# Performance work log

Measured on AMD Instinct MI355X. Metric: run time of the kernel, lower is better.

The kernel has to match this reference:

```python
import jax, jax.numpy as jnp
import numpy as np

B, S, D, H, DH = 2, 2048, 1024, 16, 64
LN_EPS = 1e-5

def _layernorm(x, g, b):
    mu = jnp.mean(x, axis=-1, keepdims=True)
    var = jnp.mean(jnp.square(x - mu), axis=-1, keepdims=True)
    return (x - mu) * jax.lax.rsqrt(var + LN_EPS) * g + b

def setup_inputs() -> dict:
    key = jax.random.key(0)
    ks = jax.random.split(key, 12)
    s = 0.02
    return {
        'x': jax.random.normal(ks[0], (B, S, D), jnp.float32),
        'attention_mask': jnp.zeros((B, S), jnp.bool_),
        'Wq': jax.random.normal(ks[1], (H, D, DH), jnp.float32) * s,
        'bq': jnp.zeros((H, DH), jnp.float32),
        'Wk': jax.random.normal(ks[2], (H, D, DH), jnp.float32) * s,
        'bk': jnp.zeros((H, DH), jnp.float32),
        'Wv': jax.random.normal(ks[3], (H, D, DH), jnp.float32) * s,
        'bv': jnp.zeros((H, DH), jnp.float32),
        'ln_g': jnp.ones((D,), jnp.float32),
        'ln_b': jnp.zeros((D,), jnp.float32),
        'W1': jax.random.normal(ks[4], (D, 4 * D), jnp.float32) * s,
        'b1': jnp.zeros((4 * D,), jnp.float32),
        'W2': jax.random.normal(ks[5], (4 * D, D), jnp.float32) * s,
        'b2': jnp.zeros((D,), jnp.float32),
    }

def reference(x, attention_mask, Wq, bq, Wk, bk, Wv, bv, ln_g, ln_b, W1, b1, W2, b2):
    # NOTE: source has a typo bug ('attentoin_score'), so the attention_mask is
    # computed-then-discarded; softmax is applied to the UNMASKED scaled scores.
    dh = Wq.shape[-1]
    q = jnp.einsum('bsd,hde->bhse', x, Wq) + bq[:, None, :]  # [B,H,S,dh]
    k = jnp.einsum('bsd,hde->bhse', x, Wk) + bk[:, None, :]
    v = jnp.einsum('bsd,hde->bhse', x, Wv) + bv[:, None, :]
    scores = jnp.einsum('bhse,bhte->bhst', q, k) / jnp.sqrt(jnp.float32(dh))
    attn = jax.nn.softmax(scores, axis=-1)
    o = jnp.einsum('bhst,bhte->bhse', attn, v)  # [B,H,S,dh]
    b_, h_, s_, e_ = o.shape
    # concat heads along last dim == transpose then reshape
    mha = jnp.transpose(o, (0, 2, 1, 3)).reshape(b_, s_, h_ * e_)
    h1 = _layernorm(x + mha, ln_g, ln_b)
    ffn = jax.nn.relu(h1 @ W1 + b1) @ W2 + b2
    return _layernorm(h1 + ffn, ln_g, ln_b)
```

## Files before the change

kernel.cpp:

```cpp
#include <hip/hip_runtime.h>

#define DEVI __device__ __forceinline__

typedef __attribute__((ext_vector_type(8))) __bf16 bf16x8;
typedef __attribute__((ext_vector_type(4))) float f32x4;
typedef __attribute__((ext_vector_type(4))) unsigned short u16x4;
typedef __attribute__((ext_vector_type(8))) unsigned short u16x8;

static DEVI unsigned short f2bf(float f) {
  unsigned int i = __float_as_uint(f);
  i += 0x7fffu + ((i >> 16) & 1u);
  return (unsigned short)(i >> 16);
}

static DEVI unsigned short f2bfh(float f) {
  union { __bf16 h; unsigned short u; } c;
  c.h = (__bf16)f;
  return c.u;
}

static DEVI float bf2f(unsigned short u) {
  return __uint_as_float((unsigned int)u << 16);
}

static DEVI f32x4 mfma16x16x32(bf16x8 a, bf16x8 b, f32x4 c) {
  return __builtin_amdgcn_mfma_f32_16x16x32_bf16(a, b, c, 0, 0, 0);
}

static DEVI void async_ld16(const void* g, void* lds) {
  __builtin_amdgcn_global_load_lds(
      (const __attribute__((address_space(1))) void*)g,
      (__attribute__((address_space(3))) void*)lds, 16, 0, 0);
}

template <int OUT_MODE, bool RELU>
static DEVI void gemm256_core(const unsigned short* __restrict__ A, int lda,
                              const unsigned short* __restrict__ Bt, int ldb,
                              int m0, int n0, const float* __restrict__ bias,
                              void* __restrict__ Cp, int ldc,
                              const float* __restrict__ bq,
                              const float* __restrict__ bk,
                              const float* __restrict__ bv,
                              unsigned short* __restrict__ qo,
                              unsigned short* __restrict__ ko,
                              unsigned short* __restrict__ vo) {
  constexpr int NKT = 16;
  __shared__ __align__(16) unsigned short As[2][16384];
  __shared__ __align__(16) unsigned short Bs[2][16384];

  const int tid = threadIdx.x;
  const int w = tid >> 6, l = tid & 63;
  const int lr = l & 15, lq = l >> 4;
  const int wm = w >> 2, wn = w & 3;

  const int srow = tid >> 3;
  const int scol = ((tid & 7) ^ (srow & 7)) << 3;
  const unsigned short* sA = A + (size_t)(m0 + srow) * lda + scol;
  const unsigned short* sB = Bt + (size_t)(n0 + srow) * ldb + scol;
  unsigned short* dA = &As[0][0] + w * 512;
  unsigned short* dB = &Bs[0][0] + w * 512;

  auto stA = [&](int c, int h, int kb) {
    const unsigned short* s = sA + (size_t)h * 128 * lda + kb;
    unsigned short* d = dA + c * 16384 + h * 8192;
    async_ld16(s, d);
    async_ld16(s + (size_t)64 * lda, d + 4096);
  };
  auto stB = [&](int c, int h, int kb) {
    const unsigned short* s = sB + (size_t)h * 128 * ldb + kb;
    unsigned short* d = dB + c * 16384 + h * 8192;
    async_ld16(s, d);
    async_ld16(s + (size_t)64 * ldb, d + 4096);
  };

  stA(0, 0, 0); stB(0, 0, 0); stB(0, 1, 0); stA(0, 1, 0);
  stA(1, 0, 64); stB(1, 0, 64); stB(1, 1, 64);

  f32x4 acc[8][4];
#pragma unroll
  for (int i = 0; i < 8; ++i)
#pragma unroll
    for (int j = 0; j < 4; ++j) acc[i][j] = (f32x4){0.f, 0.f, 0.f, 0.f};

  const int frow = wm * 16 + lr;
  const int brow = wn * 16 + lr;
  const int g0 = (lq ^ (lr & 7)) << 3;
  const int g1 = ((4 + lq) ^ (lr & 7)) << 3;

  bf16x8 af[4][2], bf[2][2][2];

  auto mfma_quad = [&](int qm, int qn) {
    __builtin_amdgcn_s_setprio(1);
#pragma unroll
    for (int m = 0; m < 4; ++m)
#pragma unroll
      for (int n = 0; n < 2; ++n) {
        f32x4 t = acc[qm * 4 + m][qn * 2 + n];
        t = mfma16x16x32(af[m][0], bf[qn][n][0], t);
        t = mfma16x16x32(af[m][1], bf[qn][n][1], t);
        acc[qm * 4 + m][qn * 2 + n] = t;
      }
    __builtin_amdgcn_s_setprio(0);
  };

  asm volatile("s_waitcnt vmcnt(6)");
  __builtin_amdgcn_sched_barrier(0);
  __builtin_amdgcn_s_barrier();

  for (int kt = 0; kt < NKT; ++kt) {
    __builtin_amdgcn_sched_barrier(0);
    const int c = kt & 1;
    const unsigned short* Ac = &As[c][0];
    const unsigned short* Bc = &Bs[c][0];
    const int kb1 = (kt + 1) * 64, kb2 = (kt + 2) * 64;

#pragma unroll
    for (int m = 0; m < 4; ++m) {
      const unsigned short* p = Ac + (frow + m * 32) * 64;
      af[m][0] = *(const bf16x8*)(p + g0);
      af[m][1] = *(const bf16x8*)(p + g1);
    }
#pragma unroll
    for (int n = 0; n < 2; ++n) {
      const unsigned short* p = Bc + (brow + n * 64) * 64;
      bf[0][n][0] = *(const bf16x8*)(p + g0);
      bf[0][n][1] = *(const bf16x8*)(p + g1);
    }
    if (kt + 1 < NKT) stA(c ^ 1, 1, kb1);
    __builtin_amdgcn_s_barrier();
    asm volatile("s_waitcnt lgkmcnt(0)");
    __builtin_amdgcn_sched_barrier(0);
    mfma_quad(0, 0);
    __builtin_amdgcn_s_barrier();

#pragma unroll
    for (int n = 0; n < 2; ++n) {
      const unsigned short* p = Bc + (128 + brow + n * 64) * 64;
      bf[1][n][0] = *(const bf16x8*)(p + g0);
      bf[1][n][1] = *(const bf16x8*)(p + g1);
    }
    if (kt + 2 < NKT) stA(c, 0, kb2);
    __builtin_amdgcn_s_barrier();
    asm volatile("s_waitcnt lgkmcnt(0)");
    __builtin_amdgcn_sched_barrier(0);
    mfma_quad(0, 1);
    __builtin_amdgcn_s_barrier();

#pragma unroll
    for (int m = 0; m < 4; ++m) {
      const unsigned short* p = Ac + (128 + frow + m * 32) * 64;
      af[m][0] = *(const bf16x8*)(p + g0);
      af[m][1] = *(const bf16x8*)(p + g1);
    }
    if (kt + 2 < NKT) stB(c, 0, kb2);
    __builtin_amdgcn_s_barrier();
    asm volatile("s_waitcnt lgkmcnt(0)");
    __builtin_amdgcn_sched_barrier(0);
    mfma_quad(1, 0);
    __builtin_amdgcn_s_barrier();

    if (kt + 2 < NKT) stB(c, 1, kb2);
    __builtin_amdgcn_s_barrier();
    asm volatile("s_waitcnt lgkmcnt(0)");
    __builtin_amdgcn_sched_barrier(0);
    mfma_quad(1, 1);
    if (kt < NKT - 2)
      asm volatile("s_waitcnt vmcnt(6)");
    else
      asm volatile("s_waitcnt vmcnt(0)");
    __builtin_amdgcn_sched_barrier(0);
    __builtin_amdgcn_s_barrier();
  }

#pragma unroll
  for (int qm = 0; qm < 2; ++qm)
#pragma unroll
    for (int m = 0; m < 4; ++m) {
      const int grow = m0 + qm * 128 + wm * 16 + m * 32 + lq * 4;
#pragma unroll
      for (int qn = 0; qn < 2; ++qn)
#pragma unroll
        for (int n = 0; n < 2; ++n) {
          const int gcol = n0 + qn * 128 + wn * 16 + n * 64 + lr;
          const f32x4 av = acc[qm * 4 + m][qn * 2 + n];
          if (OUT_MODE == 2) {
            const int which = gcol >> 10;
            const int h = (gcol >> 6) & 15;
            const int e = gcol & 63;
            const float* bp = (which == 0) ? bq : (which == 1) ? bk : bv;
            const float bvv = bp[gcol & 1023];
#pragma unroll
            for (int r = 0; r < 4; ++r) {
              const int row = grow + r;
              const int b_ = row >> 11, s_ = row & 2047;
              const size_t base = (size_t)((b_ << 4) + h) * 131072;
              const float val = av[r] + bvv;
              if (which == 0) {
                qo[base + (size_t)s_ * 64 + e] = f2bf(val);
              } else if (which == 1) {
                const int o = e >> 3;
                const int pos = (((o ^ (s_ & 7)) << 3) | (e & 7));
                ko[base + (size_t)s_ * 64 + pos] = f2bf(val * 0.18033688011112f);
              } else {
                const int t = s_ >> 6, k64 = s_ & 63;
                const int kap = (k64 & 15) * 4 + (k64 >> 4);
                const int pos = (((kap >> 3) ^ (e & 7)) << 3) | (kap & 7);
                vo[base + (size_t)e * 2048 + t * 64 + pos] = f2bf(val);
              }
            }
          } else if (OUT_MODE == 3) {
#pragma unroll
            for (int r = 0; r < 4; ++r)
              ((unsigned short*)Cp)[(size_t)(grow + r) * ldc + gcol] =
                  f2bf(av[r]);
          } else {
            const float bvv = bias[gcol];
#pragma unroll
            for (int r = 0; r < 4; ++r) {
              float val = av[r] + bvv;
              if (RELU) val = fmaxf(val, 0.f);
              ((unsigned short*)Cp)[(size_t)(grow + r) * ldc + gcol] = f2bf(val);
            }
          }
        }
    }
}

__global__ __launch_bounds__(512, 2) void k_gemm_qkv(
    const unsigned short* __restrict__ xb, const unsigned short* __restrict__ Wt,
    const float* __restrict__ bq, const float* __restrict__ bk,
    const float* __restrict__ bv, unsigned short* __restrict__ qo,
    unsigned short* __restrict__ ko, unsigned short* __restrict__ vo) {
  const int bid = blockIdx.x;
  const int xcd = bid & 7, idx = bid >> 3;
  const int mt = (xcd >> 1) * 4 + idx / 6;
  const int nt = (xcd & 1) * 6 + idx % 6;
  gemm256_core<2, false>(xb, 1024, Wt, 1024, mt * 256, nt * 256, nullptr,
                         nullptr, 0, bq, bk, bv, qo, ko, vo);
}

__global__ __launch_bounds__(512, 2) void k_ffn1(
    const unsigned short* __restrict__ h1b, const unsigned short* __restrict__ W1t,
    const float* __restrict__ b1, unsigned short* __restrict__ f1) {
  const int bid = blockIdx.x;
  const int xcd = bid & 7, idx = bid >> 3;
  const int mt = (xcd >> 1) * 4 + (idx >> 3);
  const int nt = (xcd & 1) * 8 + (idx & 7);
  gemm256_core<1, true>(h1b, 1024, W1t, 1024, mt * 256, nt * 256, b1, f1, 4096,
                        nullptr, nullptr, nullptr, nullptr, nullptr, nullptr);
}

__global__ __launch_bounds__(512, 2) void k_ffn2(
    const unsigned short* __restrict__ f1, const unsigned short* __restrict__ W2t,
    unsigned short* __restrict__ pbase) {
  const int z = blockIdx.z;
  unsigned short* p = pbase + (size_t)z * 4194304;
  const int bid = blockIdx.x;
  const int xcd = bid & 7, idx = bid >> 3;
  const int mt = xcd * 2 + (idx >> 2);
  const int nt = idx & 3;
  gemm256_core<3, false>(f1 + z * 1024, 4096, W2t + z * 1024, 4096, mt * 256,
                         nt * 256, nullptr, p, 1024, nullptr, nullptr, nullptr,
                         nullptr, nullptr, nullptr);
}

static DEVI void tr64(const float* __restrict__ s, int sld,
                      unsigned short* __restrict__ d, int dld) {
  __shared__ float t[64][65];
  const int tr = threadIdx.x >> 4;
  const int tc4 = (threadIdx.x & 15) * 4;
#pragma unroll
  for (int i = 0; i < 4; ++i) {
    f32x4 v = *(const f32x4*)(s + (size_t)(i * 16 + tr) * sld + tc4);
#pragma unroll
    for (int j = 0; j < 4; ++j) t[i * 16 + tr][tc4 + j] = v[j];
  }
  __syncthreads();
#pragma unroll
  for (int i = 0; i < 4; ++i) {
    const int c = i * 16 + tr;
    u16x4 pk;
#pragma unroll
    for (int j = 0; j < 4; ++j) pk[j] = f2bf(t[tc4 + j][c]);
    *(u16x4*)(d + (size_t)c * dld + tc4) = pk;
  }
}

__global__ __launch_bounds__(256) void k_prep(
    const float* __restrict__ x, const float* __restrict__ Wq,
    const float* __restrict__ Wk, const float* __restrict__ Wv,
    const float* __restrict__ W1, const float* __restrict__ W2,
    unsigned short* __restrict__ xb, unsigned short* __restrict__ wqkvt,
    unsigned short* __restrict__ w1t, unsigned short* __restrict__ w2t) {
  const int bid = blockIdx.x;
  if (bid < 1024) {
    const size_t i0 = ((size_t)bid * 256 + threadIdx.x) * 16;
#pragma unroll
    for (int c = 0; c < 4; ++c) {
      f32x4 v = *(const f32x4*)(x + i0 + c * 4);
      u16x4 pk;
#pragma unroll
      for (int j = 0; j < 4; ++j) pk[j] = f2bf(v[j]);
      *(u16x4*)(xb + i0 + c * 4) = pk;
    }
  } else if (bid < 1792) {
    const int t = bid - 1024;
    const int bx = t & 15, by = t >> 4;
    const int which = by >> 4, h = by & 15;
    const float* W = (which == 0) ? Wq : (which == 1) ? Wk : Wv;
    const float* s = W + (size_t)h * 65536;
    unsigned short* d = wqkvt + (size_t)(which * 1024 + h * 64) * 1024;
    const int r0 = bx * 64;
    tr64(s + (size_t)r0 * 64, 64, d + r0, 1024);
  } else if (bid < 2816) {
    const int t = bid - 1792;
    const int bx = t & 15, by = t >> 4;
    const int r0 = bx * 64, c0 = by * 64;
    tr64(W1 + (size_t)r0 * 4096 + c0, 4096, w1t + (size_t)c0 * 1024 + r0, 1024);
  } else {
    const int t = bid - 2816;
    const int bx = t & 63, by = t >> 6;
    const int r0 = bx * 64, c0 = by * 64;
    tr64(W2 + (size_t)r0 * 1024 + c0, 1024, w2t + (size_t)c0 * 4096 + r0, 4096);
  }
}

__global__ __launch_bounds__(512) void k_attn(
    const unsigned short* __restrict__ q, const unsigned short* __restrict__ ks,
    const unsigned short* __restrict__ vp, unsigned short* __restrict__ mha) {
  const int bid = blockIdx.x;
  const int bh = (bid & 7) * 4 + ((bid >> 3) >> 4);
  const int qt = (bid >> 3) & 15;
  const int b = bh >> 4, h = bh & 15;
  const int tid = threadIdx.x;
  const int w = tid >> 6, l = tid & 63;
  const int lr = l & 15, lq = l >> 4, l7 = lr & 7;

  __shared__ __align__(16) unsigned short Ks[2][64 * 64];
  __shared__ __align__(16) unsigned short Vt[2][64 * 64];
  __shared__ __align__(16) unsigned short Ps[8][16][72];

  const size_t bho = (size_t)bh * 131072;
  const int q0 = qt * 128 + w * 16;

  bf16x8 qf0, qf1;
  {
    const unsigned short* qp = q + bho + (size_t)(q0 + lr) * 64 + lq * 8;
    qf0 = *(const bf16x8*)qp;
    qf1 = *(const bf16x8*)(qp + 32);
  }

  f32x4 l_acc[4];
  f32x4 o[4];
#pragma unroll
  for (int i = 0; i < 4; ++i) {
    l_acc[i] = (f32x4){0.f, 0.f, 0.f, 0.f};
    o[i] = (f32x4){0.f, 0.f, 0.f, 0.f};
  }

  const unsigned short* kg = ks + bho;
  const unsigned short* vg = vp + bho;
  const int srow = l >> 3, scol = (l & 7) * 8;
  const int r0 = w * 8;

  async_ld16(kg + (size_t)(r0 + srow) * 64 + scol, &Ks[0][r0 * 64]);
  async_ld16(vg + (size_t)(r0 + srow) * 2048 + scol, &Vt[0][r0 * 64]);
  __syncthreads();

  for (int kt = 0; kt < 32; ++kt) {
    const int cur = kt & 1, nxt = cur ^ 1;
    if (kt + 1 < 32) {
      const int k1 = (kt + 1) * 64;
      async_ld16(kg + (size_t)(k1 + r0 + srow) * 64 + scol, &Ks[nxt][r0 * 64]);
      async_ld16(vg + (size_t)(r0 + srow) * 2048 + k1 + scol, &Vt[nxt][r0 * 64]);
    }

    bf16x8 kf[4][2];
#pragma unroll
    for (int ct = 0; ct < 4; ++ct)
#pragma unroll
      for (int hh = 0; hh < 2; ++hh)
        kf[ct][hh] = *(const bf16x8*)&Ks[cur][(ct * 16 + lr) * 64 +
                                             (((hh << 2) | lq) ^ l7) * 8];
    f32x4 s[4];
#pragma unroll
    for (int ct = 0; ct < 4; ++ct) {
      f32x4 t = {0.f, 0.f, 0.f, 0.f};
      t = mfma16x16x32(qf0, kf[ct][0], t);
      t = mfma16x16x32(qf1, kf[ct][1], t);
      s[ct] = t;
    }

#pragma unroll
    for (int r = 0; r < 4; ++r) {
      f32x4 pe;
#pragma unroll
      for (int ct = 0; ct < 4; ++ct)
        pe[ct] = __builtin_amdgcn_exp2f(s[ct][r]);
      l_acc[r] += pe;
      u16x4 pk;
#pragma unroll
      for (int ct = 0; ct < 4; ++ct) pk[ct] = f2bfh(pe[ct]);
      *(u16x4*)&Ps[w][lq * 4 + r][lr * 4] = pk;
    }
    __asm__ volatile("" ::: "memory");

    bf16x8 vf[4][2];
#pragma unroll
    for (int dt = 0; dt < 4; ++dt)
#pragma unroll
      for (int hh = 0; hh < 2; ++hh)
        vf[dt][hh] = *(const bf16x8*)&Vt[cur][(dt * 16 + lr) * 64 +
                                             (((hh << 2) | lq) ^ l7) * 8];
    bf16x8 pf0 = *(const bf16x8*)&Ps[w][lr][lq * 8];
    bf16x8 pf1 = *(const bf16x8*)&Ps[w][lr][32 + lq * 8];
#pragma unroll
    for (int dt = 0; dt < 4; ++dt) {
      o[dt] = mfma16x16x32(pf0, vf[dt][0], o[dt]);
      o[dt] = mfma16x16x32(pf1, vf[dt][1], o[dt]);
    }
    __syncthreads();
  }

#pragma unroll
  for (int r = 0; r < 4; ++r) {
    f32x4 la = l_acc[r];
    float sd = la[0] + la[1] + la[2] + la[3];
    sd += __shfl_xor(sd, 1);
    sd += __shfl_xor(sd, 2);
    sd += __shfl_xor(sd, 4);
    sd += __shfl_xor(sd, 8);
    const float inv = 1.f / sd;
    unsigned short* op =
        mha + ((size_t)b * 2048 + q0 + lq * 4 + r) * 1024 + h * 64 + lr;
    op[0] = f2bfh(o[0][r] * inv);
    op[16] = f2bfh(o[1][r] * inv);
    op[32] = f2bfh(o[2][r] * inv);
    op[48] = f2bfh(o[3][r] * inv);
  }
}

__global__ __launch_bounds__(256) void k_add_ln(const float* __restrict__ a,
                                                const unsigned short* __restrict__ b,
                                                const float* __restrict__ g,
                                                const float* __restrict__ be,
                                                unsigned short* __restrict__ outb) {
  const int row = blockIdx.x;
  const int tid = threadIdx.x;
  const size_t base = (size_t)row * 1024 + tid * 4;
  f32x4 va = *(const f32x4*)(a + base);
  u16x4 ub = *(const u16x4*)(b + base);
  f32x4 xx;
  float s = 0.f, q = 0.f;
#pragma unroll
  for (int i = 0; i < 4; ++i) {
    xx[i] = va[i] + bf2f(ub[i]);
    s += xx[i];
    q += xx[i] * xx[i];
  }
#pragma unroll
  for (int off = 1; off < 64; off <<= 1) {
    s += __shfl_xor(s, off);
    q += __shfl_xor(q, off);
  }
  __shared__ float ss[4], qs[4];
  const int w = tid >> 6;
  if ((tid & 63) == 0) { ss[w] = s; qs[w] = q; }
  __syncthreads();
  s = ss[0] + ss[1] + ss[2] + ss[3];
  q = qs[0] + qs[1] + qs[2] + qs[3];
  const float mean = s * (1.f / 1024.f);
  const float var = q * (1.f / 1024.f) - mean * mean;
  const float rstd = rsqrtf(var + 1e-5f);
  f32x4 vg = *(const f32x4*)(g + tid * 4);
  f32x4 vbe = *(const f32x4*)(be + tid * 4);
  u16x4 pk;
#pragma unroll
  for (int i = 0; i < 4; ++i)
    pk[i] = f2bf((xx[i] - mean) * rstd * vg[i] + vbe[i]);
  *(u16x4*)(outb + base) = pk;
}

__global__ __launch_bounds__(256) void k_add_ln4(
    const unsigned short* __restrict__ h1b, const unsigned short* __restrict__ pb,
    const float* __restrict__ cb, const float* __restrict__ g,
    const float* __restrict__ be, float* __restrict__ out) {
  const int row = blockIdx.x;
  const int tid = threadIdx.x;
  const size_t base = (size_t)row * 1024 + tid * 4;
  u16x4 uh = *(const u16x4*)(h1b + base);
  u16x4 up[4];
#pragma unroll
  for (int z = 0; z < 4; ++z)
    up[z] = *(const u16x4*)(pb + base + (size_t)z * 4194304);
  f32x4 vcb = *(const f32x4*)(cb + tid * 4);
  f32x4 xx;
  float s = 0.f, q = 0.f;
#pragma unroll
  for (int i = 0; i < 4; ++i) {
    float v = bf2f(uh[i]) + vcb[i];
#pragma unroll
    for (int z = 0; z < 4; ++z) v += bf2f(up[z][i]);
    xx[i] = v;
    s += v;
    q += v * v;
  }
#pragma unroll
  for (int off = 1; off < 64; off <<= 1) {
    s += __shfl_xor(s, off);
    q += __shfl_xor(q, off);
  }
  __shared__ float ss[4], qs[4];
  const int w = tid >> 6;
  if ((tid & 63) == 0) { ss[w] = s; qs[w] = q; }
  __syncthreads();
  s = ss[0] + ss[1] + ss[2] + ss[3];
  q = qs[0] + qs[1] + qs[2] + qs[3];
  const float mean = s * (1.f / 1024.f);
  const float var = q * (1.f / 1024.f) - mean * mean;
  const float rstd = rsqrtf(var + 1e-5f);
  f32x4 vg = *(const f32x4*)(g + tid * 4);
  f32x4 vbe = *(const f32x4*)(be + tid * 4);
  f32x4 ov;
#pragma unroll
  for (int i = 0; i < 4; ++i) ov[i] = (xx[i] - mean) * rstd * vg[i] + vbe[i];
  *(f32x4*)(out + base) = ov;
}

extern "C" void kernel_launch(void* const* d_in, const int* in_sizes, int n_in,
                              void* d_out, int out_size, void* d_ws,
                              size_t ws_size, hipStream_t stream) {
  const float* x = (const float*)d_in[0];
  const float* Wq = (const float*)d_in[2];
  const float* bq = (const float*)d_in[3];
  const float* Wk = (const float*)d_in[4];
  const float* bk = (const float*)d_in[5];
  const float* Wv = (const float*)d_in[6];
  const float* bv = (const float*)d_in[7];
  const float* lg = (const float*)d_in[8];
  const float* lb = (const float*)d_in[9];
  const float* W1 = (const float*)d_in[10];
  const float* b1 = (const float*)d_in[11];
  const float* W2 = (const float*)d_in[12];
  const float* b2 = (const float*)d_in[13];

  char* ws = (char*)d_ws;
  const size_t MB = 1024 * 1024;
  unsigned short* qb = (unsigned short*)(ws + 0);
  unsigned short* kb = (unsigned short*)(ws + 8 * MB);
  unsigned short* vp = (unsigned short*)(ws + 16 * MB);
  unsigned short* f1 = (unsigned short*)(ws + 0);
  unsigned short* xb = (unsigned short*)(ws + 32 * MB);
  unsigned short* pb = (unsigned short*)(ws + 32 * MB);
  unsigned short* mha = (unsigned short*)(ws + 40 * MB);
  unsigned short* h1b = (unsigned short*)(ws + 64 * MB);
  unsigned short* wqkvt = (unsigned short*)(ws + 72 * MB);
  unsigned short* w1t = (unsigned short*)(ws + 78 * MB);
  unsigned short* w2t = (unsigned short*)(ws + 86 * MB);

  k_prep<<<dim3(3840), 256, 0, stream>>>(x, Wq, Wk, Wv, W1, W2, xb, wqkvt, w1t,
                                         w2t);
  k_gemm_qkv<<<dim3(192), 512, 0, stream>>>(xb, wqkvt, bq, bk, bv, qb, kb, vp);
  k_attn<<<dim3(512), 512, 0, stream>>>(qb, kb, vp, mha);
  k_add_ln<<<dim3(4096), 256, 0, stream>>>(x, mha, lg, lb, h1b);
  k_ffn1<<<dim3(256), 512, 0, stream>>>(h1b, w1t, b1, f1);
  k_ffn2<<<dim3(64, 1, 4), 512, 0, stream>>>(f1, w2t, pb);
  k_add_ln4<<<dim3(4096), 256, 0, stream>>>(h1b, pb, b2, lg, lb, (float*)d_out);
}
```

Measured before the change: 305.7 us.

## Replace QKV GEMM with simple 128x128-tile kernel using more blocks

The QKV projection moves off the 256x256 double-buffered, software-pipelined GEMM core onto a new simpler core with 128x128 tiles, 256 threads, a single LDS buffer and K-step 32. The grid grows from 192 to 768 blocks, which spreads the work across more CUs and lowers per-block register and LDS use. In exchange the new core drops the async-load pipelining, the LDS swizzle and the XCD-aware tile mapping, so it risks more barrier stalls and LDS bank conflicts per K-step.

```diff
diff --git a/kernel.cpp b/kernel.cpp
--- a/kernel.cpp
+++ b/kernel.cpp
@@ -33,10 +33,12 @@
       (__attribute__((address_space(3))) void*)lds, 16, 0, 0);
 }
 
-template <int OUT_MODE, bool RELU>
-static DEVI void gemm256_core(const unsigned short* __restrict__ A, int lda,
+
+template <int BN, int OUT_MODE, bool RELU>
+static DEVI void gemm_bt_core(const unsigned short* __restrict__ A, int lda,
                               const unsigned short* __restrict__ Bt, int ldb,
-                              int m0, int n0, const float* __restrict__ bias,
+                              int K, int m0, int n0,
+                              const float* __restrict__ bias,
                               void* __restrict__ Cp, int ldc,
                               const float* __restrict__ bq,
                               const float* __restrict__ bk,
@@ -44,6 +46,115 @@
                               unsigned short* __restrict__ qo,
                               unsigned short* __restrict__ ko,
                               unsigned short* __restrict__ vo) {
+  constexpr int MT = (BN == 128) ? 4 : 2;
+  constexpr int NT = 4;
+  __shared__ __align__(16) unsigned short As[128 * 32];
+  __shared__ __align__(16) unsigned short Bs[BN * 32];
+
+  const int tid = threadIdx.x;
+  const int w = tid >> 6, l = tid & 63;
+  const int lr = l & 15, lq = l >> 4;
+  const int wm0 = (BN == 128) ? ((w >> 1) * 64) : (w * 32);
+  const int wn0 = (BN == 128) ? ((w & 1) * 64) : 0;
+  const int lrow = l >> 2;
+  const int lcol = (l & 3) * 8;
+
+  f32x4 acc[MT][NT];
+#pragma unroll
+  for (int i = 0; i < MT; ++i)
+#pragma unroll
+    for (int j = 0; j < NT; ++j) acc[i][j] = (f32x4){0.f, 0.f, 0.f, 0.f};
+
+  for (int kb = 0; kb < K; kb += 32) {
+#pragma unroll
+    for (int p = 0; p < 2; ++p) {
+      const int r0 = p * 64 + w * 16;
+      async_ld16(A + (size_t)(m0 + r0 + lrow) * lda + kb + lcol, As + r0 * 32);
+    }
+#pragma unroll
+    for (int p = 0; p < BN / 64; ++p) {
+      const int r0 = p * 64 + w * 16;
+      async_ld16(Bt + (size_t)(n0 + r0 + lrow) * ldb + kb + lcol, Bs + r0 * 32);
+    }
+    __syncthreads();
+
+    bf16x8 af[MT], bfr[NT];
+#pragma unroll
+    for (int mt = 0; mt < MT; ++mt)
+      af[mt] = *(const bf16x8*)(As + (wm0 + mt * 16 + lr) * 32 + lq * 8);
+#pragma unroll
+    for (int nt = 0; nt < NT; ++nt)
+      bfr[nt] = *(const bf16x8*)(Bs + (wn0 + nt * 16 + lr) * 32 + lq * 8);
+#pragma unroll
+    for (int mt = 0; mt < MT; ++mt)
+#pragma unroll
+      for (int nt = 0; nt < NT; ++nt)
+        acc[mt][nt] = mfma16x16x32(af[mt], bfr[nt], acc[mt][nt]);
+    __syncthreads();
+  }
+
+#pragma unroll
+  for (int mt = 0; mt < MT; ++mt) {
+    const int grow = m0 + wm0 + mt * 16 + lq * 4;
+#pragma unroll
+    for (int nt = 0; nt < NT; ++nt) {
+      const int gcol = n0 + wn0 + nt * 16 + lr;
+      if (OUT_MODE == 2) {
+        const int which = gcol >> 10;
+        const int h = (gcol >> 6) & 15;
+        const int e = gcol & 63;
+        const float* bp = (which == 0) ? bq : (which == 1) ? bk : bv;
+        const float bvv = bp[gcol & 1023];
+#pragma unroll
+        for (int r = 0; r < 4; ++r) {
+          const int row = grow + r;
+          const int b_ = row >> 11, s_ = row & 2047;
+          const size_t base = (size_t)((b_ << 4) + h) * 131072;
+          const float val = acc[mt][nt][r] + bvv;
+          if (which == 0) {
+            qo[base + (size_t)s_ * 64 + e] = f2bf(val);
+          } else if (which == 1) {
+            const int o = e >> 3;
+            const int pos = (((o ^ (s_ & 7)) << 3) | (e & 7));
+            ko[base + (size_t)s_ * 64 + pos] = f2bf(val * 0.18033688011112f);
+          } else {
+            const int t = s_ >> 6, k64 = s_ & 63;
+            const int kap = (k64 & 15) * 4 + (k64 >> 4);
+            const int pos = (((kap >> 3) ^ (e & 7)) << 3) | (kap & 7);
+            vo[base + (size_t)e * 2048 + t * 64 + pos] = f2bf(val);
+          }
+        }
+      } else {
+        const float bvv = bias ? bias[gcol] : 0.f;
+#pragma unroll
+        for (int r = 0; r < 4; ++r) {
+          float val = acc[mt][nt][r] + bvv;
+          if (RELU) val = fmaxf(val, 0.f);
+          if (OUT_MODE == 1)
+            ((unsigned short*)Cp)[(size_t)(grow + r) * ldc + gcol] = f2bf(val);
+          else
+            ((float*)Cp)[(size_t)(grow + r) * ldc + gcol] = val;
+        }
+      }
+    }
+  }
+}
+
+__global__ __launch_bounds__(256) void k_gemm_qkv(
+    const unsigned short* __restrict__ xb, const unsigned short* __restrict__ Wt,
+    const float* __restrict__ bq, const float* __restrict__ bk,
+    const float* __restrict__ bv, unsigned short* __restrict__ qo,
+    unsigned short* __restrict__ ko, unsigned short* __restrict__ vo) {
+  gemm_bt_core<128, 2, false>(xb, 1024, Wt, 1024, 1024, blockIdx.x * 128,
+                              blockIdx.y * 128, nullptr, nullptr, 0, bq, bk, bv,
+                              qo, ko, vo);
+}
+
+template <int OUT_MODE, bool RELU>
+static DEVI void gemm256_core(const unsigned short* __restrict__ A, int lda,
+                              const unsigned short* __restrict__ Bt, int ldb,
+                              int m0, int n0, const float* __restrict__ bias,
+                              void* __restrict__ Cp, int ldc) {
   constexpr int NKT = 16;
   __shared__ __align__(16) unsigned short As[2][16384];
   __shared__ __align__(16) unsigned short Bs[2][16384];
@@ -183,32 +294,7 @@
         for (int n = 0; n < 2; ++n) {
           const int gcol = n0 + qn * 128 + wn * 16 + n * 64 + lr;
           const f32x4 av = acc[qm * 4 + m][qn * 2 + n];
-          if (OUT_MODE == 2) {
-            const int which = gcol >> 10;
-            const int h = (gcol >> 6) & 15;
-            const int e = gcol & 63;
-            const float* bp = (which == 0) ? bq : (which == 1) ? bk : bv;
-            const float bvv = bp[gcol & 1023];
-#pragma unroll
-            for (int r = 0; r < 4; ++r) {
-              const int row = grow + r;
-              const int b_ = row >> 11, s_ = row & 2047;
-              const size_t base = (size_t)((b_ << 4) + h) * 131072;
-              const float val = av[r] + bvv;
-              if (which == 0) {
-                qo[base + (size_t)s_ * 64 + e] = f2bf(val);
-              } else if (which == 1) {
-                const int o = e >> 3;
-                const int pos = (((o ^ (s_ & 7)) << 3) | (e & 7));
-                ko[base + (size_t)s_ * 64 + pos] = f2bf(val * 0.18033688011112f);
-              } else {
-                const int t = s_ >> 6, k64 = s_ & 63;
-                const int kap = (k64 & 15) * 4 + (k64 >> 4);
-                const int pos = (((kap >> 3) ^ (e & 7)) << 3) | (kap & 7);
-                vo[base + (size_t)e * 2048 + t * 64 + pos] = f2bf(val);
-              }
-            }
-          } else if (OUT_MODE == 3) {
+          if (OUT_MODE == 3) {
 #pragma unroll
             for (int r = 0; r < 4; ++r)
               ((unsigned short*)Cp)[(size_t)(grow + r) * ldc + gcol] =
@@ -226,19 +312,6 @@
     }
 }
 
-__global__ __launch_bounds__(512, 2) void k_gemm_qkv(
-    const unsigned short* __restrict__ xb, const unsigned short* __restrict__ Wt,
-    const float* __restrict__ bq, const float* __restrict__ bk,
-    const float* __restrict__ bv, unsigned short* __restrict__ qo,
-    unsigned short* __restrict__ ko, unsigned short* __restrict__ vo) {
-  const int bid = blockIdx.x;
-  const int xcd = bid & 7, idx = bid >> 3;
-  const int mt = (xcd >> 1) * 4 + idx / 6;
-  const int nt = (xcd & 1) * 6 + idx % 6;
-  gemm256_core<2, false>(xb, 1024, Wt, 1024, mt * 256, nt * 256, nullptr,
-                         nullptr, 0, bq, bk, bv, qo, ko, vo);
-}
-
 __global__ __launch_bounds__(512, 2) void k_ffn1(
     const unsigned short* __restrict__ h1b, const unsigned short* __restrict__ W1t,
     const float* __restrict__ b1, unsigned short* __restrict__ f1) {
@@ -246,8 +319,7 @@
   const int xcd = bid & 7, idx = bid >> 3;
   const int mt = (xcd >> 1) * 4 + (idx >> 3);
   const int nt = (xcd & 1) * 8 + (idx & 7);
-  gemm256_core<1, true>(h1b, 1024, W1t, 1024, mt * 256, nt * 256, b1, f1, 4096,
-                        nullptr, nullptr, nullptr, nullptr, nullptr, nullptr);
+  gemm256_core<1, true>(h1b, 1024, W1t, 1024, mt * 256, nt * 256, b1, f1, 4096);
 }
 
 __global__ __launch_bounds__(512, 2) void k_ffn2(
@@ -260,8 +332,7 @@
   const int mt = xcd * 2 + (idx >> 2);
   const int nt = idx & 3;
   gemm256_core<3, false>(f1 + z * 1024, 4096, W2t + z * 1024, 4096, mt * 256,
-                         nt * 256, nullptr, p, 1024, nullptr, nullptr, nullptr,
-                         nullptr, nullptr, nullptr);
+                         nt * 256, nullptr, p, 1024);
 }
 
 static DEVI void tr64(const float* __restrict__ s, int sld,
@@ -560,7 +631,7 @@
 
   k_prep<<<dim3(3840), 256, 0, stream>>>(x, Wq, Wk, Wv, W1, W2, xb, wqkvt, w1t,
                                          w2t);
-  k_gemm_qkv<<<dim3(192), 512, 0, stream>>>(xb, wqkvt, bq, bk, bv, qb, kb, vp);
+  k_gemm_qkv<<<dim3(32, 24), 256, 0, stream>>>(xb, wqkvt, bq, bk, bv, qb, kb, vp);
   k_attn<<<dim3(512), 512, 0, stream>>>(qb, kb, vp, mha);
   k_add_ln<<<dim3(4096), 256, 0, stream>>>(x, mha, lg, lb, h1b);
   k_ffn1<<<dim3(256), 512, 0, stream>>>(h1b, w1t, b1, f1);
```

New measurement: 294.7 us. 3.6% less time.
